# Kernel optimization log

Hardware: AMD Instinct MI355X
Metric: run time of the kernel (lower is better)

## Reference

```python
import jax, jax.numpy as jnp
import numpy as np

S = 3072      # total tokens across all images
DIM = 1280    # hidden_size
H = 16        # num_heads
HD = DIM // H # head_dim = 80
NSEG = 6      # number of images (cu_seqlens has NSEG+1 entries)


def _rotate_half(x):
    x1, x2 = jnp.split(x, 2, axis=-1)
    return jnp.concatenate([-x2, x1], axis=-1)


def setup_inputs() -> dict:
    key = jax.random.key(0)
    ks = jax.random.split(key, 12)
    hidden_states = jax.random.normal(ks[0], (S, DIM), jnp.float32)
    # realistic vision rotary embedding: half-dim inv_freq, repeated to head_dim
    inv_freq = 1.0 / (10000.0 ** (jnp.arange(0, HD // 2, dtype=jnp.float32) / (HD // 2)))
    freqs = jnp.arange(S, dtype=jnp.float32)[:, None] * inv_freq[None, :]  # [S, HD/2]
    emb = jnp.concatenate([freqs, freqs], axis=-1)  # [S, HD]
    cos = jnp.cos(emb)
    sin = jnp.sin(emb)
    sc = 0.02
    wq = jax.random.normal(ks[1], (DIM, DIM), jnp.float32) * sc
    bq = jax.random.normal(ks[2], (DIM,), jnp.float32) * sc
    wk = jax.random.normal(ks[3], (DIM, DIM), jnp.float32) * sc
    bk = jax.random.normal(ks[4], (DIM,), jnp.float32) * sc
    wv = jax.random.normal(ks[5], (DIM, DIM), jnp.float32) * sc
    bv = jax.random.normal(ks[6], (DIM,), jnp.float32) * sc
    wo = jax.random.normal(ks[7], (DIM, DIM), jnp.float32) * sc
    bo = jax.random.normal(ks[8], (DIM,), jnp.float32) * sc
    cu_seqlens = (jnp.arange(NSEG + 1, dtype=jnp.int32) * (S // NSEG))  # [0,512,...,3072]
    return dict(hidden_states=hidden_states, cos=cos, sin=sin,
                wq=wq, bq=bq, wk=wk, bk=bk, wv=wv, bv=bv, wo=wo, bo=bo,
                cu_seqlens=cu_seqlens)


def reference(hidden_states, cos, sin, wq, bq, wk, bk, wv, bv, wo, bo, cu_seqlens):
    seq_length = hidden_states.shape[0]
    scaling = HD ** (-0.5)
    # QKV projections (torch Linear: x @ W.T + b)
    q = (hidden_states @ wq.T + bq).reshape(seq_length, H, HD)
    k = (hidden_states @ wk.T + bk).reshape(seq_length, H, HD)
    v = (hidden_states @ wv.T + bv).reshape(seq_length, H, HD)
    # apply_rotary_pos_emb_vision: cos/sin [S, HD] broadcast over head axis
    c = cos[:, None, :]
    s = sin[:, None, :]
    q = q * c + _rotate_half(q) * s
    k = k * c + _rotate_half(k) * s
    # block-diagonal (per-image) attention via segment mask
    seg = jnp.searchsorted(cu_seqlens[1:], jnp.arange(seq_length), side='right')
    mask = seg[:, None] == seg[None, :]  # [S, S] bool
    scores = jnp.einsum('shd,thd->hst', q, k) * scaling  # [H, S, S]
    scores = jnp.where(mask[None, :, :], scores, jnp.finfo(scores.dtype).min)
    attn = jax.nn.softmax(scores, axis=-1)
    out = jnp.einsum('hst,thd->shd', attn, v).reshape(seq_length, DIM)
    return out @ wo.T + bo
```

## Files before the change

kernel.cpp:

```cpp
#include <hip/hip_runtime.h>
#include <hip/hip_bf16.h>
#include <hip/hip_fp16.h>
#include <cstdint>
#include <cstddef>

typedef _Float16 f16;
typedef f16 f16x2 __attribute__((ext_vector_type(2)));
typedef f16 f16x4 __attribute__((ext_vector_type(4)));
typedef f16 f16x8 __attribute__((ext_vector_type(8)));
typedef float f32x4 __attribute__((ext_vector_type(4)));

#define S_LEN 3072
#define DIM 1280
#define NH 16
#define HD 80
#define SEG 512

#define MFMA16F(a, b, c) __builtin_amdgcn_mfma_f32_16x16x32_f16((a), (b), (c), 0, 0, 0)

__device__ __forceinline__ void gl2lds16(const void* g, void* l) {
    __builtin_amdgcn_global_load_lds(
        (const __attribute__((address_space(1))) unsigned int*)g,
        (__attribute__((address_space(3))) unsigned int*)l, 16, 0, 0);
}

__device__ __forceinline__ unsigned int pack2(float a, float b) {
    f16x2 t = {(f16)a, (f16)b};
    union { f16x2 v; unsigned int u; } c;
    c.v = t;
    return c.u;
}

__global__ __launch_bounds__(256) void cvt_kernel(
    const float* __restrict__ hs,
    const float* __restrict__ wq, const float* __restrict__ wk,
    const float* __restrict__ wv, const float* __restrict__ wo,
    f16* __restrict__ hs16,
    f16* __restrict__ wq16, f16* __restrict__ wk16,
    f16* __restrict__ wv16, f16* __restrict__ wo16)
{
    const int m = blockIdx.y;
    const float* src; f16* dst; int n4;
    if (m == 0)      { src = hs; dst = hs16; n4 = S_LEN * DIM / 4; }
    else if (m == 1) { src = wq; dst = wq16; n4 = DIM * DIM / 4; }
    else if (m == 2) { src = wk; dst = wk16; n4 = DIM * DIM / 4; }
    else if (m == 3) { src = wv; dst = wv16; n4 = DIM * DIM / 4; }
    else             { src = wo; dst = wo16; n4 = DIM * DIM / 4; }
    int idx = blockIdx.x * 256 + threadIdx.x;
    if (idx >= n4) return;
    f32x4 v = *(const f32x4*)(src + (size_t)idx * 4);
    f16x4 o;
#pragma unroll
    for (int e = 0; e < 4; ++e) o[e] = (f16)v[e];
    *(f16x4*)(dst + (size_t)idx * 4) = o;
}

__global__ __launch_bounds__(256) void gemm_f16_kernel(
    const f16* __restrict__ A,
    const f16* __restrict__ W0, const f16* __restrict__ W1, const f16* __restrict__ W2,
    const float* __restrict__ b0, const float* __restrict__ b1, const float* __restrict__ b2,
    f16* __restrict__ O0, f16* __restrict__ O1, f16* __restrict__ O2)
{
    const int mode = blockIdx.z;
    const f16* W = (mode == 1) ? W1 : (mode == 2) ? W2 : W0;
    const float* bias = (mode == 1) ? b1 : (mode == 2) ? b2 : b0;

    __shared__ __align__(16) f16 As[128 * 32];
    __shared__ __align__(16) f16 Bs[128 * 32];

    const int tid = threadIdx.x;
    const int lane = tid & 63;
    const int lane15 = tid & 15;
    const int quad = lane >> 4;
    const int w = tid >> 6;
    const int wm = (w >> 1) * 64;
    const int wn = (w & 1) * 64;
    const int m0 = blockIdx.x * 128;
    const int n0 = blockIdx.y * 128;

    const int srow = w * 32 + (lane >> 2);
    const int scol = (lane & 3) * 8;
    const f16* gA0 = A + (size_t)(m0 + srow) * DIM + scol;
    const f16* gA1 = A + (size_t)(m0 + srow + 16) * DIM + scol;
    const f16* gB0 = W + (size_t)(n0 + srow) * DIM + scol;
    const f16* gB1 = W + (size_t)(n0 + srow + 16) * DIM + scol;
    f16* lA0 = As + (w * 32) * 32;
    f16* lA1 = As + (w * 32 + 16) * 32;
    f16* lB0 = Bs + (w * 32) * 32;
    f16* lB1 = Bs + (w * 32 + 16) * 32;

    f32x4 acc[4][4];
#pragma unroll
    for (int i = 0; i < 4; ++i)
#pragma unroll
        for (int j = 0; j < 4; ++j)
            acc[i][j] = (f32x4){0.f, 0.f, 0.f, 0.f};

    for (int kt = 0; kt < DIM / 32; ++kt) {
        __syncthreads();
        gl2lds16(gA0 + kt * 32, lA0);
        gl2lds16(gA1 + kt * 32, lA1);
        gl2lds16(gB0 + kt * 32, lB0);
        gl2lds16(gB1 + kt * 32, lB1);
        __syncthreads();

        f16x8 fa[4], fb[4];
#pragma unroll
        for (int i = 0; i < 4; ++i)
            fa[i] = *(const f16x8*)(As + (wm + i * 16 + lane15) * 32 + quad * 8);
#pragma unroll
        for (int j = 0; j < 4; ++j)
            fb[j] = *(const f16x8*)(Bs + (wn + j * 16 + lane15) * 32 + quad * 8);
#pragma unroll
        for (int i = 0; i < 4; ++i)
#pragma unroll
            for (int j = 0; j < 4; ++j)
                acc[i][j] = MFMA16F(fa[i], fb[j], acc[i][j]);
    }

    float bvv[4];
#pragma unroll
    for (int j = 0; j < 4; ++j)
        bvv[j] = bias[n0 + wn + j * 16 + lane15];

    f16* O = (mode == 0) ? O0 : (mode == 1) ? O1 : O2;
#pragma unroll
    for (int i = 0; i < 4; ++i)
#pragma unroll
        for (int j = 0; j < 4; ++j)
#pragma unroll
            for (int r = 0; r < 4; ++r) {
                int row = m0 + wm + i * 16 + quad * 4 + r;
                int col = n0 + wn + j * 16 + lane15;
                O[(size_t)row * DIM + col] = (f16)(acc[i][j][r] + bvv[j]);
            }
}

__global__ __launch_bounds__(256) void gemm_out_kernel(
    const f16* __restrict__ A, const f16* __restrict__ W,
    const float* __restrict__ bias, float* __restrict__ OF)
{
    __shared__ __align__(16) f16 As[64 * 32];
    __shared__ __align__(16) f16 Bs[128 * 32];

    const int tid = threadIdx.x;
    const int lane = tid & 63;
    const int lane15 = tid & 15;
    const int quad = lane >> 4;
    const int w = tid >> 6;
    const int wn = w * 32;
    const int m0 = blockIdx.x * 64;
    const int n0 = blockIdx.y * 128;

    const int srA = w * 16 + (lane >> 2);
    const int srB = w * 32 + (lane >> 2);
    const int scol = (lane & 3) * 8;
    const f16* gA0 = A + (size_t)(m0 + srA) * DIM + scol;
    const f16* gB0 = W + (size_t)(n0 + srB) * DIM + scol;
    const f16* gB1 = W + (size_t)(n0 + srB + 16) * DIM + scol;
    f16* lA0 = As + (w * 16) * 32;
    f16* lB0 = Bs + (w * 32) * 32;
    f16* lB1 = Bs + (w * 32 + 16) * 32;

    f32x4 acc[4][2];
#pragma unroll
    for (int i = 0; i < 4; ++i)
#pragma unroll
        for (int j = 0; j < 2; ++j)
            acc[i][j] = (f32x4){0.f, 0.f, 0.f, 0.f};

    for (int kt = 0; kt < DIM / 32; ++kt) {
        __syncthreads();
        gl2lds16(gA0 + kt * 32, lA0);
        gl2lds16(gB0 + kt * 32, lB0);
        gl2lds16(gB1 + kt * 32, lB1);
        __syncthreads();

        f16x8 fa[4], fb[2];
#pragma unroll
        for (int i = 0; i < 4; ++i)
            fa[i] = *(const f16x8*)(As + (i * 16 + lane15) * 32 + quad * 8);
#pragma unroll
        for (int j = 0; j < 2; ++j)
            fb[j] = *(const f16x8*)(Bs + (wn + j * 16 + lane15) * 32 + quad * 8);
#pragma unroll
        for (int i = 0; i < 4; ++i)
#pragma unroll
            for (int j = 0; j < 2; ++j)
                acc[i][j] = MFMA16F(fa[i], fb[j], acc[i][j]);
    }

    float bvv[2];
#pragma unroll
    for (int j = 0; j < 2; ++j)
        bvv[j] = bias[n0 + wn + j * 16 + lane15];

#pragma unroll
    for (int i = 0; i < 4; ++i)
#pragma unroll
        for (int j = 0; j < 2; ++j)
#pragma unroll
            for (int r = 0; r < 4; ++r) {
                int row = m0 + i * 16 + quad * 4 + r;
                int col = n0 + wn + j * 16 + lane15;
                OF[(size_t)row * DIM + col] = acc[i][j][r] + bvv[j];
            }
}

__global__ __launch_bounds__(256) void prep_kernel(
    f16* __restrict__ qb, f16* __restrict__ kb,
    const float* __restrict__ cosb, const float* __restrict__ sinb,
    const f16* __restrict__ v, f16* __restrict__ vT)
{
    __shared__ __align__(16) f16 Ls[128 * 128];
    const int tid = threadIdx.x;
    if (blockIdx.x < 1920) {
        int idx = blockIdx.x * 256 + tid;
        int c = idx % 5;
        int t = idx / 5;
        int h = t & 15; t >>= 4;
        int s = t % S_LEN;
        int which = t / S_LEN;
        f16* buf = which ? kb : qb;
        float scale = which ? 1.0f : 0.11180339887498948f;
        int j = c * 8;
        f32x4 ca = *(const f32x4*)(cosb + s * HD + j);
        f32x4 cb = *(const f32x4*)(cosb + s * HD + j + 4);
        f32x4 sna = *(const f32x4*)(sinb + s * HD + j);
        f32x4 snb = *(const f32x4*)(sinb + s * HD + j + 4);
        size_t base = (size_t)s * DIM + h * HD + j;
        f16x8 x1 = *(f16x8*)(buf + base);
        f16x8 x2 = *(f16x8*)(buf + base + 40);
        f16x8 o1, o2;
#pragma unroll
        for (int e = 0; e < 8; ++e) {
            float ce = (e < 4) ? ca[e] : cb[e - 4];
            float se = (e < 4) ? sna[e] : snb[e - 4];
            float a = (float)x1[e], b = (float)x2[e];
            o1[e] = (f16)((a * ce - b * se) * scale);
            o2[e] = (f16)((b * ce + a * se) * scale);
        }
        *(f16x8*)(buf + base) = o1;
        *(f16x8*)(buf + base + 40) = o2;
    } else {
        int bid = blockIdx.x - 1920;
        const int h = bid / 24;
        const int s0 = (bid - h * 24) * 128;
#pragma unroll
        for (int c = tid; c < 1280; c += 256) {
            int r = c / 10;
            int ch = c - r * 10;
            int chs = ch ^ ((r >> 3) & 7);
            *(f16x8*)(Ls + r * 128 + chs * 8) =
                *(const f16x8*)(v + (size_t)(s0 + r) * DIM + h * HD + ch * 8);
        }
        __syncthreads();
#pragma unroll
        for (int c = tid; c < 1280; c += 256) {
            int d = c >> 4;
            int sc = c & 15;
            f16x8 ov;
#pragma unroll
            for (int e = 0; e < 8; ++e) {
                int s = sc * 8 + e;
                ov[e] = Ls[s * 128 + (((d >> 3) ^ (sc & 7)) * 8) + (d & 7)];
            }
            *(f16x8*)(vT + (size_t)(h * HD + d) * S_LEN + s0 + sc * 8) = ov;
        }
    }
}

__global__ __launch_bounds__(256) void attn_kernel(
    const f16* __restrict__ q, const f16* __restrict__ k,
    const f16* __restrict__ vT, f16* __restrict__ o)
{
    const int h = blockIdx.x;
    const int g = blockIdx.y;
    const int qc = blockIdx.z;
    const int tid = threadIdx.x;
    const int lane15 = tid & 15;
    const int quad = (tid & 63) >> 4;
    const int w = tid >> 6;
    const int qbase = g * SEG + qc * 64;
    const int qrow = qbase + w * 16 + lane15;

    __shared__ __align__(16) f16 Ks[128 * 88];
    __shared__ __align__(16) f16 Vt[80 * 128];

    f16x8 zf;
#pragma unroll
    for (int e = 0; e < 8; ++e) zf[e] = (f16)0.0f;

    f16x8 fq[3];
#pragma unroll
    for (int kc = 0; kc < 3; ++kc) {
        if (kc == 2 && quad >= 2) fq[kc] = zf;
        else fq[kc] = *(const f16x8*)(q + (size_t)qrow * DIM + h * HD + kc * 32 + quad * 8);
    }

    float m_run = -1e30f, l_run = 0.f;
    f32x4 Oa[5];
#pragma unroll
    for (int dt = 0; dt < 5; ++dt) Oa[dt] = (f32x4){0.f, 0.f, 0.f, 0.f};

    for (int kt = 0; kt < 4; ++kt) {
        __syncthreads();
        const int kb = g * SEG + kt * 128;
#pragma unroll
        for (int c = tid; c < 1280; c += 256) {
            int r = c / 10;
            int c8 = (c - r * 10) * 8;
            *(f16x8*)(Ks + r * 88 + c8) =
                *(const f16x8*)(k + (size_t)(kb + r) * DIM + h * HD + c8);
        }
#pragma unroll
        for (int c = tid; c < 1280; c += 256) {
            int d = c >> 4;
            int sc = c & 15;
            *(f16x8*)(Vt + d * 128 + (sc ^ (d & 7)) * 8) =
                *(const f16x8*)(vT + (size_t)(h * HD + d) * S_LEN + kb + sc * 8);
        }
        __syncthreads();

        f32x4 sa[8];
#pragma unroll
        for (int nt = 0; nt < 8; ++nt) sa[nt] = (f32x4){0.f, 0.f, 0.f, 0.f};
#pragma unroll
        for (int kc = 0; kc < 3; ++kc) {
#pragma unroll
            for (int nt = 0; nt < 8; ++nt) {
                f16x8 fk;
                if (kc == 2 && quad >= 2) fk = zf;
                else fk = *(const f16x8*)(Ks + (nt * 16 + lane15) * 88 + kc * 32 + quad * 8);
                sa[nt] = MFMA16F(fk, fq[kc], sa[nt]);
            }
        }

        float mt = -1e30f;
#pragma unroll
        for (int nt = 0; nt < 8; ++nt)
#pragma unroll
            for (int r = 0; r < 4; ++r) mt = fmaxf(mt, sa[nt][r]);
        mt = fmaxf(mt, __shfl_xor(mt, 16, 64));
        mt = fmaxf(mt, __shfl_xor(mt, 32, 64));

        float mn = fmaxf(m_run, mt);
        float alpha = __expf(m_run - mn);
        m_run = mn;
        float lt = 0.f;
        unsigned int pp[8][2];
#pragma unroll
        for (int nt = 0; nt < 8; ++nt) {
            float p0 = __expf(sa[nt][0] - mn);
            float p1 = __expf(sa[nt][1] - mn);
            float p2 = __expf(sa[nt][2] - mn);
            float p3 = __expf(sa[nt][3] - mn);
            lt += (p0 + p1) + (p2 + p3);
            pp[nt][0] = pack2(p0, p1);
            pp[nt][1] = pack2(p2, p3);
        }
        lt += __shfl_xor(lt, 16, 64);
        lt += __shfl_xor(lt, 32, 64);
        l_run = l_run * alpha + lt;

#pragma unroll
        for (int dt = 0; dt < 5; ++dt)
#pragma unroll
            for (int r = 0; r < 4; ++r) Oa[dt][r] *= alpha;

        const int srcA = ((quad & 1) * 2) * 16 + lane15;
        const int srcB = srcA + 16;
        const bool hi = quad >= 2;
#pragma unroll
        for (int kc2 = 0; kc2 < 4; ++kc2) {
            unsigned int e0 = __shfl((int)pp[2 * kc2][0], srcA, 64);
            unsigned int e1 = __shfl((int)pp[2 * kc2][1], srcA, 64);
            unsigned int e2 = __shfl((int)pp[2 * kc2][0], srcB, 64);
            unsigned int e3 = __shfl((int)pp[2 * kc2][1], srcB, 64);
            unsigned int o0 = __shfl((int)pp[2 * kc2 + 1][0], srcA, 64);
            unsigned int o1 = __shfl((int)pp[2 * kc2 + 1][1], srcA, 64);
            unsigned int o2 = __shfl((int)pp[2 * kc2 + 1][0], srcB, 64);
            unsigned int o3 = __shfl((int)pp[2 * kc2 + 1][1], srcB, 64);
            union { unsigned int u[4]; f16x8 v; } fp;
            fp.u[0] = hi ? o0 : e0;
            fp.u[1] = hi ? o1 : e1;
            fp.u[2] = hi ? o2 : e2;
            fp.u[3] = hi ? o3 : e3;
#pragma unroll
            for (int dt = 0; dt < 5; ++dt) {
                int drow = dt * 16 + lane15;
                int slot = (kc2 * 4 + quad) ^ (drow & 7);
                f16x8 fv = *(const f16x8*)(Vt + drow * 128 + slot * 8);
                Oa[dt] = MFMA16F(fv, fp.v, Oa[dt]);
            }
        }
    }

    float inv = 1.0f / l_run;
#pragma unroll
    for (int dt = 0; dt < 5; ++dt) {
        f16x4 ov;
#pragma unroll
        for (int r = 0; r < 4; ++r) ov[r] = (f16)(Oa[dt][r] * inv);
        *(f16x4*)(o + (size_t)qrow * DIM + h * HD + dt * 16 + quad * 4) = ov;
    }
}

extern "C" void kernel_launch(void* const* d_in, const int* in_sizes, int n_in,
                              void* d_out, int out_size, void* d_ws, size_t ws_size,
                              hipStream_t stream)
{
    const float* hs   = (const float*)d_in[0];
    const float* cosb = (const float*)d_in[1];
    const float* sinb = (const float*)d_in[2];
    const float* wq   = (const float*)d_in[3];
    const float* bq   = (const float*)d_in[4];
    const float* wk   = (const float*)d_in[5];
    const float* bk   = (const float*)d_in[6];
    const float* wv   = (const float*)d_in[7];
    const float* bv   = (const float*)d_in[8];
    const float* wo   = (const float*)d_in[9];
    const float* bo   = (const float*)d_in[10];

    const size_t SD = (size_t)S_LEN * DIM;
    const size_t WW = (size_t)DIM * DIM;
    f16* hs16 = (f16*)d_ws;
    f16* wq16 = hs16 + SD;
    f16* wk16 = wq16 + WW;
    f16* wv16 = wk16 + WW;
    f16* wo16 = wv16 + WW;
    f16* q16  = wo16 + WW;
    f16* k16  = q16 + SD;
    f16* v16  = k16 + SD;
    f16* ao16 = v16 + SD;
    f16* vT16 = ao16 + SD;
    float* outb = (float*)d_out;

    cvt_kernel<<<dim3(S_LEN * DIM / 4 / 256, 5), 256, 0, stream>>>(
        hs, wq, wk, wv, wo, hs16, wq16, wk16, wv16, wo16);
    gemm_f16_kernel<<<dim3(24, 10, 3), 256, 0, stream>>>(
        hs16, wq16, wk16, wv16, bq, bk, bv, q16, k16, v16);
    prep_kernel<<<2304, 256, 0, stream>>>(q16, k16, cosb, sinb, v16, vT16);
    attn_kernel<<<dim3(NH, 6, 8), 256, 0, stream>>>(q16, k16, vT16, ao16);
    gemm_out_kernel<<<dim3(48, 10), 256, 0, stream>>>(ao16, wo16, bo, outb);
}
```

Measured before the change: 219.3 us.

## Fuse V transpose into QKV GEMM epilogue and remap blocks per XCD

The QKV GEMM now writes the V projection straight into the transposed vT layout from its epilogue, using 4-element vector stores along the sequence axis. This removes the separate transpose pass and the intermediate V buffer from the prep kernel, which becomes a pure RoPE kernel. Both GEMMs now use a flattened 1D grid with a block-index remap that groups M tiles by XCD (blockIdx & 7), intended to improve L2 reuse of A tiles. The vT stores are strided by S_LEN across columns, so they coalesce less well than row-major stores.

```diff
diff --git a/kernel.cpp b/kernel.cpp
--- a/kernel.cpp
+++ b/kernel.cpp
@@ -59,9 +59,16 @@
     const f16* __restrict__ A,
     const f16* __restrict__ W0, const f16* __restrict__ W1, const f16* __restrict__ W2,
     const float* __restrict__ b0, const float* __restrict__ b1, const float* __restrict__ b2,
-    f16* __restrict__ O0, f16* __restrict__ O1, f16* __restrict__ O2)
-{
-    const int mode = blockIdx.z;
+    f16* __restrict__ O0, f16* __restrict__ O1, f16* __restrict__ vT)
+{
+    const int f = blockIdx.x;
+    const int xcd = f & 7;
+    const int idx = f >> 3;
+    const int mt = xcd * 3 + idx % 3;
+    const int yz = idx / 3;
+    const int nt = yz % 10;
+    const int mode = yz / 10;
+
     const f16* W = (mode == 1) ? W1 : (mode == 2) ? W2 : W0;
     const float* bias = (mode == 1) ? b1 : (mode == 2) ? b2 : b0;
 
@@ -75,8 +82,8 @@
     const int w = tid >> 6;
     const int wm = (w >> 1) * 64;
     const int wn = (w & 1) * 64;
-    const int m0 = blockIdx.x * 128;
-    const int n0 = blockIdx.y * 128;
+    const int m0 = mt * 128;
+    const int n0 = nt * 128;
 
     const int srow = w * 32 + (lane >> 2);
     const int scol = (lane & 3) * 8;
@@ -123,23 +130,43 @@
     for (int j = 0; j < 4; ++j)
         bvv[j] = bias[n0 + wn + j * 16 + lane15];
 
-    f16* O = (mode == 0) ? O0 : (mode == 1) ? O1 : O2;
-#pragma unroll
-    for (int i = 0; i < 4; ++i)
-#pragma unroll
-        for (int j = 0; j < 4; ++j)
-#pragma unroll
-            for (int r = 0; r < 4; ++r) {
-                int row = m0 + wm + i * 16 + quad * 4 + r;
+    if (mode == 2) {
+#pragma unroll
+        for (int i = 0; i < 4; ++i)
+#pragma unroll
+            for (int j = 0; j < 4; ++j) {
+                f16x4 ov;
+#pragma unroll
+                for (int r = 0; r < 4; ++r) ov[r] = (f16)(acc[i][j][r] + bvv[j]);
+                int row = m0 + wm + i * 16 + quad * 4;
                 int col = n0 + wn + j * 16 + lane15;
-                O[(size_t)row * DIM + col] = (f16)(acc[i][j][r] + bvv[j]);
+                *(f16x4*)(vT + (size_t)col * S_LEN + row) = ov;
             }
+    } else {
+        f16* O = (mode == 0) ? O0 : O1;
+#pragma unroll
+        for (int i = 0; i < 4; ++i)
+#pragma unroll
+            for (int j = 0; j < 4; ++j)
+#pragma unroll
+                for (int r = 0; r < 4; ++r) {
+                    int row = m0 + wm + i * 16 + quad * 4 + r;
+                    int col = n0 + wn + j * 16 + lane15;
+                    O[(size_t)row * DIM + col] = (f16)(acc[i][j][r] + bvv[j]);
+                }
+    }
 }
 
 __global__ __launch_bounds__(256) void gemm_out_kernel(
     const f16* __restrict__ A, const f16* __restrict__ W,
     const float* __restrict__ bias, float* __restrict__ OF)
 {
+    const int f = blockIdx.x;
+    const int xcd = f & 7;
+    const int idx = f >> 3;
+    const int xt = xcd * 6 + idx % 6;
+    const int yt = idx / 6;
+
     __shared__ __align__(16) f16 As[64 * 32];
     __shared__ __align__(16) f16 Bs[128 * 32];
 
@@ -149,8 +176,8 @@
     const int quad = lane >> 4;
     const int w = tid >> 6;
     const int wn = w * 32;
-    const int m0 = blockIdx.x * 64;
-    const int n0 = blockIdx.y * 128;
+    const int m0 = xt * 64;
+    const int n0 = yt * 128;
 
     const int srA = w * 16 + (lane >> 2);
     const int srB = w * 32 + (lane >> 2);
@@ -207,67 +234,37 @@
             }
 }
 
-__global__ __launch_bounds__(256) void prep_kernel(
+__global__ __launch_bounds__(256) void rope_kernel(
     f16* __restrict__ qb, f16* __restrict__ kb,
-    const float* __restrict__ cosb, const float* __restrict__ sinb,
-    const f16* __restrict__ v, f16* __restrict__ vT)
-{
-    __shared__ __align__(16) f16 Ls[128 * 128];
-    const int tid = threadIdx.x;
-    if (blockIdx.x < 1920) {
-        int idx = blockIdx.x * 256 + tid;
-        int c = idx % 5;
-        int t = idx / 5;
-        int h = t & 15; t >>= 4;
-        int s = t % S_LEN;
-        int which = t / S_LEN;
-        f16* buf = which ? kb : qb;
-        float scale = which ? 1.0f : 0.11180339887498948f;
-        int j = c * 8;
-        f32x4 ca = *(const f32x4*)(cosb + s * HD + j);
-        f32x4 cb = *(const f32x4*)(cosb + s * HD + j + 4);
-        f32x4 sna = *(const f32x4*)(sinb + s * HD + j);
-        f32x4 snb = *(const f32x4*)(sinb + s * HD + j + 4);
-        size_t base = (size_t)s * DIM + h * HD + j;
-        f16x8 x1 = *(f16x8*)(buf + base);
-        f16x8 x2 = *(f16x8*)(buf + base + 40);
-        f16x8 o1, o2;
-#pragma unroll
-        for (int e = 0; e < 8; ++e) {
-            float ce = (e < 4) ? ca[e] : cb[e - 4];
-            float se = (e < 4) ? sna[e] : snb[e - 4];
-            float a = (float)x1[e], b = (float)x2[e];
-            o1[e] = (f16)((a * ce - b * se) * scale);
-            o2[e] = (f16)((b * ce + a * se) * scale);
-        }
-        *(f16x8*)(buf + base) = o1;
-        *(f16x8*)(buf + base + 40) = o2;
-    } else {
-        int bid = blockIdx.x - 1920;
-        const int h = bid / 24;
-        const int s0 = (bid - h * 24) * 128;
-#pragma unroll
-        for (int c = tid; c < 1280; c += 256) {
-            int r = c / 10;
-            int ch = c - r * 10;
-            int chs = ch ^ ((r >> 3) & 7);
-            *(f16x8*)(Ls + r * 128 + chs * 8) =
-                *(const f16x8*)(v + (size_t)(s0 + r) * DIM + h * HD + ch * 8);
-        }
-        __syncthreads();
-#pragma unroll
-        for (int c = tid; c < 1280; c += 256) {
-            int d = c >> 4;
-            int sc = c & 15;
-            f16x8 ov;
-#pragma unroll
-            for (int e = 0; e < 8; ++e) {
-                int s = sc * 8 + e;
-                ov[e] = Ls[s * 128 + (((d >> 3) ^ (sc & 7)) * 8) + (d & 7)];
-            }
-            *(f16x8*)(vT + (size_t)(h * HD + d) * S_LEN + s0 + sc * 8) = ov;
-        }
-    }
+    const float* __restrict__ cosb, const float* __restrict__ sinb)
+{
+    int idx = blockIdx.x * 256 + threadIdx.x;
+    int c = idx % 5;
+    int t = idx / 5;
+    int h = t & 15; t >>= 4;
+    int s = t % S_LEN;
+    int which = t / S_LEN;
+    f16* buf = which ? kb : qb;
+    float scale = which ? 1.0f : 0.11180339887498948f;
+    int j = c * 8;
+    f32x4 ca = *(const f32x4*)(cosb + s * HD + j);
+    f32x4 cb = *(const f32x4*)(cosb + s * HD + j + 4);
+    f32x4 sna = *(const f32x4*)(sinb + s * HD + j);
+    f32x4 snb = *(const f32x4*)(sinb + s * HD + j + 4);
+    size_t base = (size_t)s * DIM + h * HD + j;
+    f16x8 x1 = *(f16x8*)(buf + base);
+    f16x8 x2 = *(f16x8*)(buf + base + 40);
+    f16x8 o1, o2;
+#pragma unroll
+    for (int e = 0; e < 8; ++e) {
+        float ce = (e < 4) ? ca[e] : cb[e - 4];
+        float se = (e < 4) ? sna[e] : snb[e - 4];
+        float a = (float)x1[e], b = (float)x2[e];
+        o1[e] = (f16)((a * ce - b * se) * scale);
+        o2[e] = (f16)((b * ce + a * se) * scale);
+    }
+    *(f16x8*)(buf + base) = o1;
+    *(f16x8*)(buf + base + 40) = o2;
 }
 
 __global__ __launch_bounds__(256) void attn_kernel(
@@ -431,16 +428,15 @@
     f16* wo16 = wv16 + WW;
     f16* q16  = wo16 + WW;
     f16* k16  = q16 + SD;
-    f16* v16  = k16 + SD;
-    f16* ao16 = v16 + SD;
-    f16* vT16 = ao16 + SD;
+    f16* vT16 = k16 + SD;
+    f16* ao16 = vT16 + SD;
     float* outb = (float*)d_out;
 
     cvt_kernel<<<dim3(S_LEN * DIM / 4 / 256, 5), 256, 0, stream>>>(
         hs, wq, wk, wv, wo, hs16, wq16, wk16, wv16, wo16);
-    gemm_f16_kernel<<<dim3(24, 10, 3), 256, 0, stream>>>(
-        hs16, wq16, wk16, wv16, bq, bk, bv, q16, k16, v16);
-    prep_kernel<<<2304, 256, 0, stream>>>(q16, k16, cosb, sinb, v16, vT16);
+    gemm_f16_kernel<<<720, 256, 0, stream>>>(
+        hs16, wq16, wk16, wv16, bq, bk, bv, q16, k16, vT16);
+    rope_kernel<<<1920, 256, 0, stream>>>(q16, k16, cosb, sinb);
     attn_kernel<<<dim3(NH, 6, 8), 256, 0, stream>>>(q16, k16, vT16, ao16);
-    gemm_out_kernel<<<dim3(48, 10), 256, 0, stream>>>(ao16, wo16, bo, outb);
-}
+    gemm_out_kernel<<<480, 256, 0, stream>>>(ao16, wo16, bo, outb);
+}
```

Result: no change. 217.7 us (-0.7%).
